# Kernel optimization log

Hardware: AMD Instinct MI355X
Metric: run time of the kernel (lower is better)

Reference implementation:

```python
import jax, jax.numpy as jnp
import numpy as np

TOP_K = 2  # num_experts_per_tok


def setup_inputs() -> dict:
    key = jax.random.key(0)
    ks = jax.random.split(key, 5)
    B, S, D, M, E = 4, 2048, 2048, 2048, 8
    x = jax.random.normal(ks[0], (B, S, D), dtype=jnp.float32)
    gate_kernel = jax.random.normal(ks[1], (D, E), dtype=jnp.float32) / np.sqrt(D)
    wi_0 = jax.random.normal(ks[2], (E, D, M), dtype=jnp.float32) / np.sqrt(D)
    wi_1 = jax.random.normal(ks[3], (E, D, M), dtype=jnp.float32) / np.sqrt(D)
    wo = jax.random.normal(ks[4], (E, M, D), dtype=jnp.float32) / np.sqrt(M)
    return {"x": x, "gate_kernel": gate_kernel, "wi_0": wi_0, "wi_1": wi_1, "wo": wo}


def reference(x, gate_kernel, wi_0, wi_1, wo):
    E = gate_kernel.shape[-1]
    # Gate logits: (B, S, E)
    gate_logits = jnp.einsum("bsd,de->bse", x, gate_kernel)
    # Top-k routing, then softmax over the selected experts' logits
    top_k_weights, top_k_indices = jax.lax.top_k(gate_logits, TOP_K)
    top_k_weights = jax.nn.softmax(top_k_weights.astype(jnp.float32), axis=-1).astype(x.dtype)
    # Dense combine weights per expert: (B, S, E)
    combine_w = jnp.sum(
        jax.nn.one_hot(top_k_indices, E, dtype=x.dtype) * top_k_weights[..., None], axis=-2
    )
    # Grouped GEMM (dense-masked form, as in MaxText dense_matmul path)
    h0 = jnp.einsum("bsd,edm->bsem", x, wi_0)  # (B, S, E, M)
    h1 = jnp.einsum("bsd,edm->bsem", x, wi_1)
    h = jax.nn.silu(h0) * h1 * combine_w[..., None]
    out = jnp.einsum("bsem,emd->bsd", h, wo)  # (B, S, D)
    return out
```

## Files before the change

kernel.cpp:

```cpp
#include <hip/hip_runtime.h>
#include <hip/hip_bf16.h>
#include <stdint.h>

#define TT   8192
#define DD   2048
#define MM   2048
#define NE   8

typedef float f32x4 __attribute__((ext_vector_type(4)));
typedef short s16x8 __attribute__((ext_vector_type(8)));
typedef unsigned int u32;
typedef unsigned long long u64;

static __device__ __forceinline__ short f2bf(float f) {
  __hip_bfloat16 h = __float2bfloat16(f);
  short s;
  __builtin_memcpy(&s, &h, 2);
  return s;
}
static __device__ __forceinline__ float bf2f(short s) {
  u32 u = ((u32)(unsigned short)s) << 16;
  float f;
  __builtin_memcpy(&f, &u, 4);
  return f;
}

static __device__ __forceinline__ void gload_lds16(const short* g, short* lds) {
  __builtin_amdgcn_global_load_lds(
      (const __attribute__((address_space(1))) u32*)g,
      (__attribute__((address_space(3))) u32*)lds, 16, 0, 0);
}

#define VM2()  asm volatile("s_waitcnt vmcnt(2)" ::: "memory")
#define VM0()  asm volatile("s_waitcnt vmcnt(0)" ::: "memory")
#define LG0()  asm volatile("s_waitcnt lgkmcnt(0)" ::: "memory")
#define BAR()  __builtin_amdgcn_s_barrier()

__global__ __launch_bounds__(256) void tcvt_kernel(
    const float* __restrict__ w0, const float* __restrict__ w1, const float* __restrict__ w2,
    short* __restrict__ o0, short* __restrict__ o1, short* __restrict__ o2) {
  __shared__ short tile[64][65];
  const int bz = blockIdx.z;
  const float* in; short* out;
  if (bz < 8)       { in = w0; out = o0; }
  else if (bz < 16) { in = w1; out = o1; }
  else              { in = w2; out = o2; }
  const int ex = bz & 7;
  const float* src = in + (size_t)ex * DD * MM;
  short* dst = out + (size_t)ex * DD * MM;
  const int r0 = blockIdx.y * 64;
  const int c0 = blockIdx.x * 64;
  const int t = threadIdx.x;
  const int rr = t >> 4, cc = (t & 15) * 4;
  #pragma unroll
  for (int i = 0; i < 4; i++) {
    int row = rr + i * 16;
    f32x4 v = *(const f32x4*)(src + (size_t)(r0 + row) * MM + c0 + cc);
    tile[cc + 0][row] = f2bf(v[0]);
    tile[cc + 1][row] = f2bf(v[1]);
    tile[cc + 2][row] = f2bf(v[2]);
    tile[cc + 3][row] = f2bf(v[3]);
  }
  __syncthreads();
  const int orow = t >> 2, c8 = (t & 3) * 16;
  s16x8 v0, v1;
  #pragma unroll
  for (int i = 0; i < 8; i++) { v0[i] = tile[orow][c8 + i]; v1[i] = tile[orow][c8 + 8 + i]; }
  short* dp = dst + (size_t)(c0 + orow) * DD + r0 + c8;
  *(s16x8*)(dp) = v0;
  *(s16x8*)(dp + 8) = v1;
}

__global__ __launch_bounds__(256) void gate_kernel(const float* __restrict__ x,
    const float* __restrict__ gk, int* __restrict__ counts,
    int* __restrict__ tkidx, float* __restrict__ tkw, short* __restrict__ xbf) {
  int t = blockIdx.x;
  const float* xr = x + (size_t)t * DD;
  const int d0 = threadIdx.x * 8;
  f32x4 a = *(const f32x4*)(xr + d0);
  f32x4 b = *(const f32x4*)(xr + d0 + 4);
  s16x8 v;
  v[0]=f2bf(a[0]); v[1]=f2bf(a[1]); v[2]=f2bf(a[2]); v[3]=f2bf(a[3]);
  v[4]=f2bf(b[0]); v[5]=f2bf(b[1]); v[6]=f2bf(b[2]); v[7]=f2bf(b[3]);
  *(s16x8*)(xbf + (size_t)t * DD + d0) = v;

  float acc[NE];
  #pragma unroll
  for (int e = 0; e < NE; e++) acc[e] = 0.f;
  #pragma unroll
  for (int j = 0; j < 8; j++) {
    float xv = (j < 4) ? a[j] : b[j - 4];
    const float* g = gk + (size_t)(d0 + j) * NE;
    #pragma unroll
    for (int e = 0; e < NE; e++) acc[e] += xv * g[e];
  }
  #pragma unroll
  for (int e = 0; e < NE; e++) {
    #pragma unroll
    for (int off = 32; off >= 1; off >>= 1)
      acc[e] += __shfl_xor(acc[e], off, 64);
  }
  __shared__ float red[4][NE];
  int wid = threadIdx.x >> 6;
  int lane = threadIdx.x & 63;
  if (lane == 0) {
    #pragma unroll
    for (int e = 0; e < NE; e++) red[wid][e] = acc[e];
  }
  __syncthreads();
  if (threadIdx.x == 0) {
    float l[NE];
    #pragma unroll
    for (int e = 0; e < NE; e++) l[e] = red[0][e] + red[1][e] + red[2][e] + red[3][e];
    int i1 = 0; float v1 = l[0];
    #pragma unroll
    for (int e = 1; e < NE; e++) if (l[e] > v1) { v1 = l[e]; i1 = e; }
    int i2 = -1; float v2 = -1e30f;
    #pragma unroll
    for (int e = 0; e < NE; e++) if (e != i1 && l[e] > v2) { v2 = l[e]; i2 = e; }
    float p = __expf(v2 - v1);
    float inv = 1.f / (1.f + p);
    tkidx[t*2]   = i1; tkidx[t*2+1] = i2;
    tkw[t*2]     = inv; tkw[t*2+1]  = p * inv;
    atomicAdd(&counts[i1], 1);
    atomicAdd(&counts[i2], 1);
  }
}

__global__ __launch_bounds__(256) void scatter_kernel(const int* __restrict__ counts,
    int* __restrict__ offsets, const int* __restrict__ tkidx,
    const float* __restrict__ tkw, int* __restrict__ ltok, float* __restrict__ lwt,
    int* __restrict__ slots) {
  const int e = blockIdx.x;
  const int tid = threadIdx.x;
  const int wid = tid >> 6, lane = tid & 63;
  __shared__ int base_s;
  __shared__ int wsum[4];
  if (tid == 0) {
    int s = 0;
    #pragma unroll
    for (int i = 0; i < NE; i++) {
      if (e == 0) offsets[i] = s;
      if (i < e) s += counts[i];
      else if (e == 0) s += counts[i];
    }
    if (e == 0) offsets[NE] = s;
    int bs = 0;
    for (int i = 0; i < e; i++) bs += counts[i];
    base_s = bs;
  }
  __syncthreads();
  int base = base_s;
  for (int it = 0; it < (TT * 2) / 256; it++) {
    int i = it * 256 + tid;
    bool m = (tkidx[i] == e);
    u64 b = __ballot(m);
    if (lane == 0) wsum[wid] = __popcll(b);
    __syncthreads();
    int pre = 0;
    #pragma unroll
    for (int w = 0; w < 4; w++) if (w < wid) pre += wsum[w];
    int tot = wsum[0] + wsum[1] + wsum[2] + wsum[3];
    int rank = __popcll(b & ((lane == 0) ? 0ull : ((1ull << lane) - 1ull)));
    if (m) {
      int dst = base + pre + rank;
      ltok[dst] = i >> 1;
      lwt[dst]  = tkw[i];
      slots[i]  = dst;
    }
    __syncthreads();
    base += tot;
  }
}

__global__ __launch_bounds__(256) void combine_kernel(const short* __restrict__ comb,
    const int* __restrict__ slots, float* __restrict__ out) {
  const int t = blockIdx.x;
  const int s0 = slots[2 * t], s1 = slots[2 * t + 1];
  const int idx = threadIdx.x;
  s16x8 a = *(const s16x8*)(comb + (size_t)s0 * DD + idx * 8);
  s16x8 b = *(const s16x8*)(comb + (size_t)s1 * DD + idx * 8);
  f32x4 o0, o1;
  #pragma unroll
  for (int j = 0; j < 4; j++) {
    o0[j] = bf2f(a[j]) + bf2f(b[j]);
    o1[j] = bf2f(a[4 + j]) + bf2f(b[4 + j]);
  }
  float* po = out + (size_t)t * DD + idx * 8;
  *(f32x4*)(po) = o0;
  *(f32x4*)(po + 4) = o1;
}

__device__ __forceinline__ void find_seg(const int* __restrict__ offsets, int tile, int bm,
                                         int& e, int& row0, int& rows, int& seg) {
  e = -1; row0 = 0; rows = 0; seg = 0;
  int accT = 0, prev = offsets[0];
  #pragma unroll
  for (int i = 0; i < NE; i++) {
    int nxt = offsets[i+1];
    int cnt = nxt - prev;
    int nt = (cnt + bm - 1) / bm;
    if (e < 0 && tile < accT + nt) { e = i; row0 = (tile - accT) * bm; rows = cnt; seg = prev; }
    accT += nt; prev = nxt;
  }
}

__device__ __forceinline__ void xcd_map(int ypx, int& tile, int& nyi) {
  const int bid = blockIdx.y * gridDim.x + blockIdx.x;
  const int xcd = bid & 7;
  const int i = bid >> 3;
  tile = i / ypx;
  nyi  = xcd * ypx + (i % ypx);
}

#define MAXT1 136

__global__ __launch_bounds__(256, 2) void gemm1_fast(
    const short* __restrict__ xbf,
    const short* __restrict__ w0t, const short* __restrict__ w1t,
    const int* __restrict__ offsets,
    const int* __restrict__ ltok, const float* __restrict__ lwt,
    short* __restrict__ hbuf) {
  __shared__ short As[128 * 64];
  __shared__ short B0s[128 * 64];
  __shared__ short B1s[128 * 64];
  __shared__ float w_s[128];

  int tile, nyi;
  xcd_map(2, tile, nyi);
  const int n0 = nyi * 128;
  int e, row0, rows, seg;
  find_seg(offsets, tile, 128, e, row0, rows, seg);
  if (e < 0) return;

  const int tid = threadIdx.x;
  const int lane = tid & 63, wid = tid >> 6;
  if (tid < 128) {
    int gr = row0 + tid;
    w_s[tid] = (gr < rows) ? lwt[seg + gr] : 0.f;
  }

  const int swz = ((lane & 7) ^ (lane >> 3)) * 8;
  const short* abase[4];
  const short* b0base[4];
  const short* b1base[4];
  #pragma unroll
  for (int c = 0; c < 4; c++) {
    int chunk = wid * 4 + c;
    int r = chunk * 8 + (lane >> 3);
    int gr = row0 + r; if (gr >= rows) gr = rows - 1;
    int tok = ltok[seg + gr];
    abase[c]  = xbf + (size_t)tok * DD + swz;
    int n = n0 + r;
    b0base[c] = w0t + ((size_t)e * MM + n) * DD + swz;
    b1base[c] = w1t + ((size_t)e * MM + n) * DD + swz;
  }

  const int wr = wid >> 1, wc = wid & 1;
  const int lr = lane & 15;
  const int kq = (lane >> 4) * 8;

  f32x4 acc0[4][4], acc1[4][4];
  #pragma unroll
  for (int i = 0; i < 4; i++)
    #pragma unroll
    for (int j = 0; j < 4; j++) { acc0[i][j] = 0.f; acc1[i][j] = 0.f; }

  for (int k0 = 0; k0 < DD; k0 += 64) {
    #pragma unroll
    for (int c = 0; c < 4; c++) {
      int chunk = wid * 4 + c;
      gload_lds16(abase[c]  + k0, As  + chunk * 512);
      gload_lds16(b0base[c] + k0, B0s + chunk * 512);
      gload_lds16(b1base[c] + k0, B1s + chunk * 512);
    }
    __syncthreads();

    #pragma unroll
    for (int ks = 0; ks < 2; ks++) {
      s16x8 a[4], b0[4], b1[4];
      #pragma unroll
      for (int mi = 0; mi < 4; mi++) {
        int row = wr * 64 + mi * 16 + lr;
        int koff = (ks * 32 + kq) ^ ((row & 7) * 8);
        a[mi] = *(const s16x8*)&As[row * 64 + koff];
      }
      #pragma unroll
      for (int ni = 0; ni < 4; ni++) {
        int row = wc * 64 + ni * 16 + lr;
        int koff = (ks * 32 + kq) ^ ((row & 7) * 8);
        b0[ni] = *(const s16x8*)&B0s[row * 64 + koff];
        b1[ni] = *(const s16x8*)&B1s[row * 64 + koff];
      }
      #pragma unroll
      for (int mi = 0; mi < 4; mi++)
        #pragma unroll
        for (int ni = 0; ni < 4; ni++) {
          acc0[mi][ni] = __builtin_amdgcn_mfma_f32_16x16x32_bf16(a[mi], b0[ni], acc0[mi][ni], 0, 0, 0);
          acc1[mi][ni] = __builtin_amdgcn_mfma_f32_16x16x32_bf16(a[mi], b1[ni], acc1[mi][ni], 0, 0, 0);
        }
    }
    __syncthreads();
  }

  const int lq = lane >> 4;
  #pragma unroll
  for (int mi = 0; mi < 4; mi++) {
    #pragma unroll
    for (int jj = 0; jj < 4; jj++) {
      int r = wr * 64 + mi * 16 + lq * 4 + jj;
      int gr = row0 + r;
      if (gr < rows) {
        float wgt = w_s[r];
        size_t hrow = (size_t)(seg + gr) * MM + n0;
        #pragma unroll
        for (int ni = 0; ni < 4; ni++) {
          int c = wc * 64 + ni * 16 + lr;
          float g = acc0[mi][ni][jj];
          float u = acc1[mi][ni][jj];
          float act = g / (1.f + __expf(-g));
          hbuf[hrow + c] = f2bf(act * u * wgt);
        }
      }
    }
  }
}

#define MAXT2 72

__global__ __launch_bounds__(512, 2) void gemm2_fast(
    const short* __restrict__ hbuf,
    const short* __restrict__ wot,
    const int* __restrict__ offsets,
    short* __restrict__ comb) {
  __shared__ short As[2][256 * 64];
  __shared__ short Bs[2][256 * 64];

  int tile, nyi;
  xcd_map(1, tile, nyi);
  const int n0 = nyi * 256;
  int e, row0, rows, seg;
  find_seg(offsets, tile, 256, e, row0, rows, seg);
  if (e < 0) return;

  const int tid = threadIdx.x;
  const int lane = tid & 63, wid = tid >> 6;
  const int srow = tid >> 3;
  const int swz = ((tid & 7) ^ (srow & 7)) * 8;

  const short* aP[2][2];
  const short* bP[2][2];
  #pragma unroll
  for (int h = 0; h < 2; h++)
    #pragma unroll
    for (int rd = 0; rd < 2; rd++) {
      int gr = row0 + h * 128 + rd * 64 + srow;
      if (gr >= rows) gr = rows - 1;
      aP[h][rd] = hbuf + (size_t)(seg + gr) * MM + swz;
      int n = n0 + h * 128 + rd * 64 + srow;
      bP[h][rd] = wot + ((size_t)e * DD + n) * MM + swz;
    }
  const short* aP00 = aP[0][0]; const short* aP01 = aP[0][1];
  const short* aP10 = aP[1][0]; const short* aP11 = aP[1][1];
  const short* bP00 = bP[0][0]; const short* bP01 = bP[0][1];
  const short* bP10 = bP[1][0]; const short* bP11 = bP[1][1];

  const int wr = wid >> 2, wn = wid & 3;
  const int lr = lane & 15;
  const int kq = (lane >> 4) * 8;
  const int lq = lane >> 4;

  f32x4 acc[8][4];
  #pragma unroll
  for (int i = 0; i < 8; i++)
    #pragma unroll
    for (int j = 0; j < 4; j++) acc[i][j] = 0.f;

  int brow_[4], bkey_[4];
  #pragma unroll
  for (int ni = 0; ni < 4; ni++) {
    brow_[ni] = wn * 64 + ni * 16 + lr;
    bkey_[ni] = (brow_[ni] & 7) * 8;
  }
  int arowL_[4], akeyL_[4], arowH_[4], akeyH_[4];
  #pragma unroll
  for (int mi = 0; mi < 4; mi++) {
    arowL_[mi] = wr * 128 + mi * 16 + lr;        akeyL_[mi] = (arowL_[mi] & 7) * 8;
    arowH_[mi] = wr * 128 + (mi + 4) * 16 + lr;  akeyH_[mi] = (arowH_[mi] & 7) * 8;
  }

  const int wofs = wid * 512;
  auto stA0 = [&](int buf, int kof) {
    short* d = &As[buf][0];
    gload_lds16(aP00 + kof, d + wofs);
    gload_lds16(aP01 + kof, d + 4096 + wofs);
  };
  auto stA1 = [&](int buf, int kof) {
    short* d = &As[buf][128 * 64];
    gload_lds16(aP10 + kof, d + wofs);
    gload_lds16(aP11 + kof, d + 4096 + wofs);
  };
  auto stB0 = [&](int buf, int kof) {
    short* d = &Bs[buf][0];
    gload_lds16(bP00 + kof, d + wofs);
    gload_lds16(bP01 + kof, d + 4096 + wofs);
  };
  auto stB1 = [&](int buf, int kof) {
    short* d = &Bs[buf][128 * 64];
    gload_lds16(bP10 + kof, d + wofs);
    gload_lds16(bP11 + kof, d + 4096 + wofs);
  };

  stA0(0, 0); stB0(0, 0); stB1(0, 0); stA1(0, 0);
  stA0(1, 64);
  VM2();
  BAR();

  const int NIT = (MM / 64) / 2;
  s16x8 av[4], bv[4], bw[4];

  for (int it = 0; it < NIT; ++it) {
    const bool pf = (it + 1 < NIT);
    const int kb  = (2 * it + 1) * 64;
    const int kna = (2 * it + 2) * 64;
    const int knb = (2 * it + 3) * 64;

    #pragma unroll
    for (int mi = 0; mi < 4; mi++) av[mi] = *(const s16x8*)&As[0][arowL_[mi] * 64 + (kq ^ akeyL_[mi])];
    #pragma unroll
    for (int ni = 0; ni < 4; ni++) bv[ni] = *(const s16x8*)&Bs[0][brow_[ni] * 64 + (kq ^ bkey_[ni])];
    stB0(1, kb);
    BAR(); LG0();
    __builtin_amdgcn_s_setprio(1);
    #pragma unroll
    for (int mi = 0; mi < 4; mi++)
      #pragma unroll
      for (int ni = 0; ni < 4; ni++)
        acc[mi][ni] = __builtin_amdgcn_mfma_f32_16x16x32_bf16(av[mi], bv[ni], acc[mi][ni], 0, 0, 0);
    __builtin_amdgcn_s_setprio(0);
    BAR();

    #pragma unroll
    for (int mi = 0; mi < 4; mi++) av[mi] = *(const s16x8*)&As[0][arowH_[mi] * 64 + (kq ^ akeyH_[mi])];
    stB1(1, kb);
    BAR(); LG0();
    __builtin_amdgcn_s_setprio(1);
    #pragma unroll
    for (int mi = 0; mi < 4; mi++)
      #pragma unroll
      for (int ni = 0; ni < 4; ni++)
        acc[mi + 4][ni] = __builtin_amdgcn_mfma_f32_16x16x32_bf16(av[mi], bv[ni], acc[mi + 4][ni], 0, 0, 0);
    __builtin_amdgcn_s_setprio(0);
    BAR();

    #pragma unroll
    for (int mi = 0; mi < 4; mi++) av[mi] = *(const s16x8*)&As[0][arowL_[mi] * 64 + ((32 + kq) ^ akeyL_[mi])];
    #pragma unroll
    for (int ni = 0; ni < 4; ni++) bw[ni] = *(const s16x8*)&Bs[0][brow_[ni] * 64 + ((32 + kq) ^ bkey_[ni])];
    stA1(1, kb);
    BAR(); LG0();
    __builtin_amdgcn_s_setprio(1);
    #pragma unroll
    for (int mi = 0; mi < 4; mi++)
      #pragma unroll
      for (int ni = 0; ni < 4; ni++)
        acc[mi][ni] = __builtin_amdgcn_mfma_f32_16x16x32_bf16(av[mi], bw[ni], acc[mi][ni], 0, 0, 0);
    __builtin_amdgcn_s_setprio(0);
    BAR();

    #pragma unroll
    for (int mi = 0; mi < 4; mi++) av[mi] = *(const s16x8*)&As[0][arowH_[mi] * 64 + ((32 + kq) ^ akeyH_[mi])];
    if (pf) stA0(0, kna);
    BAR(); LG0();
    __builtin_amdgcn_s_setprio(1);
    #pragma unroll
    for (int mi = 0; mi < 4; mi++)
      #pragma unroll
      for (int ni = 0; ni < 4; ni++)
        acc[mi + 4][ni] = __builtin_amdgcn_mfma_f32_16x16x32_bf16(av[mi], bw[ni], acc[mi + 4][ni], 0, 0, 0);
    __builtin_amdgcn_s_setprio(0);
    if (pf) { VM2(); } else { VM0(); }
    BAR();

    #pragma unroll
    for (int mi = 0; mi < 4; mi++) av[mi] = *(const s16x8*)&As[1][arowL_[mi] * 64 + (kq ^ akeyL_[mi])];
    #pragma unroll
    for (int ni = 0; ni < 4; ni++) bv[ni] = *(const s16x8*)&Bs[1][brow_[ni] * 64 + (kq ^ bkey_[ni])];
    if (pf) stB0(0, kna);
    BAR(); LG0();
    __builtin_amdgcn_s_setprio(1);
    #pragma unroll
    for (int mi = 0; mi < 4; mi++)
      #pragma unroll
      for (int ni = 0; ni < 4; ni++)
        acc[mi][ni] = __builtin_amdgcn_mfma_f32_16x16x32_bf16(av[mi], bv[ni], acc[mi][ni], 0, 0, 0);
    __builtin_amdgcn_s_setprio(0);
    BAR();

    #pragma unroll
    for (int mi = 0; mi < 4; mi++) av[mi] = *(const s16x8*)&As[1][arowH_[mi] * 64 + (kq ^ akeyH_[mi])];
    if (pf) stB1(0, kna);
    BAR(); LG0();
    __builtin_amdgcn_s_setprio(1);
    #pragma unroll
    for (int mi = 0; mi < 4; mi++)
      #pragma unroll
      for (int ni = 0; ni < 4; ni++)
        acc[mi + 4][ni] = __builtin_amdgcn_mfma_f32_16x16x32_bf16(av[mi], bv[ni], acc[mi + 4][ni], 0, 0, 0);
    __builtin_amdgcn_s_setprio(0);
    BAR();

    #pragma unroll
    for (int mi = 0; mi < 4; mi++) av[mi] = *(const s16x8*)&As[1][arowL_[mi] * 64 + ((32 + kq) ^ akeyL_[mi])];
    #pragma unroll
    for (int ni = 0; ni < 4; ni++) bw[ni] = *(const s16x8*)&Bs[1][brow_[ni] * 64 + ((32 + kq) ^ bkey_[ni])];
    if (pf) stA1(0, kna);
    BAR(); LG0();
    __builtin_amdgcn_s_setprio(1);
    #pragma unroll
    for (int mi = 0; mi < 4; mi++)
      #pragma unroll
      for (int ni = 0; ni < 4; ni++)
        acc[mi][ni] = __builtin_amdgcn_mfma_f32_16x16x32_bf16(av[mi], bw[ni], acc[mi][ni], 0, 0, 0);
    __builtin_amdgcn_s_setprio(0);
    BAR();

    #pragma unroll
    for (int mi = 0; mi < 4; mi++) av[mi] = *(const s16x8*)&As[1][arowH_[mi] * 64 + ((32 + kq) ^ akeyH_[mi])];
    if (pf) stA0(1, knb);
    BAR(); LG0();
    __builtin_amdgcn_s_setprio(1);
    #pragma unroll
    for (int mi = 0; mi < 4; mi++)
      #pragma unroll
      for (int ni = 0; ni < 4; ni++)
        acc[mi + 4][ni] = __builtin_amdgcn_mfma_f32_16x16x32_bf16(av[mi], bw[ni], acc[mi + 4][ni], 0, 0, 0);
    __builtin_amdgcn_s_setprio(0);
    if (pf) { VM2(); BAR(); }
  }

  #pragma unroll
  for (int mi = 0; mi < 8; mi++) {
    #pragma unroll
    for (int jj = 0; jj < 4; jj++) {
      int r = wr * 128 + mi * 16 + lq * 4 + jj;
      int gr = row0 + r;
      if (gr < rows) {
        size_t orow = (size_t)(seg + gr) * DD + n0;
        #pragma unroll
        for (int ni = 0; ni < 4; ni++) {
          int c = wn * 64 + ni * 16 + lr;
          comb[orow + c] = f2bf(acc[mi][ni][jj]);
        }
      }
    }
  }
}

extern "C" void kernel_launch(void* const* d_in, const int* in_sizes, int n_in,
                              void* d_out, int out_size, void* d_ws, size_t ws_size,
                              hipStream_t stream) {
  const float* x   = (const float*)d_in[0];
  const float* gk  = (const float*)d_in[1];
  const float* wi0 = (const float*)d_in[2];
  const float* wi1 = (const float*)d_in[3];
  const float* wo  = (const float*)d_in[4];
  float* out = (float*)d_out;

  char* w = (char*)d_ws;
  int*   counts  = (int*)(w);
  int*   offsets = (int*)(w + 256);
  int*   tkidx   = (int*)(w + 1024);
  float* tkw     = (float*)(w + 1024 + 65536);
  int*   ltok    = (int*)(w + 1024 + 2*65536);
  float* lwt     = (float*)(w + 1024 + 3*65536);
  int*   slots   = (int*)(w + 1024 + 4*65536);
  short* xbf  = (short*)(w + 524288);
  short* hbuf = xbf + (size_t)TT * DD;
  short* w0t  = hbuf + (size_t)2 * TT * MM;
  short* w1t  = w0t + (size_t)NE * DD * MM;
  short* wot  = w1t + (size_t)NE * DD * MM;
  short* comb = w0t;

  hipMemsetAsync(counts, 0, 64, stream);

  gate_kernel<<<TT, 256, 0, stream>>>(x, gk, counts, tkidx, tkw, xbf);
  scatter_kernel<<<NE, 256, 0, stream>>>(counts, offsets, tkidx, tkw, ltok, lwt, slots);
  tcvt_kernel<<<dim3(MM/64, DD/64, 24), 256, 0, stream>>>(wi0, wi1, wo, w0t, w1t, wot);

  gemm1_fast<<<dim3(MAXT1, MM/128), 256, 0, stream>>>(xbf, w0t, w1t, offsets, ltok, lwt, hbuf);
  gemm2_fast<<<dim3(MAXT2, DD/256), 512, 0, stream>>>(hbuf, wot, offsets, comb);
  combine_kernel<<<TT, 256, 0, stream>>>(comb, slots, out);
}
```

Before: 890.7 us.

## Fold wo weight conversion into gemm1 launch to overlap with GEMM

The fp32-to-bf16 transpose-convert of wo moves out of the standalone conversion kernel and into extra blocks appended to the gemm1 grid. Those blocks use the A shared-memory buffer as a transpose tile and then return. The aim is to overlap the memory-bound wo conversion with the compute-bound first grouped GEMM, which also runs partly as a tail for early-exiting gemm1 blocks. The 2D grid becomes 1D, so the XCD mapping is recomputed inline. Since conversion blocks come after the GEMM blocks in the grid, they may only get scheduled late and could still compete for bandwidth and slots.

```diff
diff --git a/kernel.cpp b/kernel.cpp
--- a/kernel.cpp
+++ b/kernel.cpp
@@ -36,15 +36,13 @@
 #define LG0()  asm volatile("s_waitcnt lgkmcnt(0)" ::: "memory")
 #define BAR()  __builtin_amdgcn_s_barrier()
 
-__global__ __launch_bounds__(256) void tcvt_kernel(
-    const float* __restrict__ w0, const float* __restrict__ w1, const float* __restrict__ w2,
-    short* __restrict__ o0, short* __restrict__ o1, short* __restrict__ o2) {
+__global__ __launch_bounds__(256) void tcvt01_kernel(
+    const float* __restrict__ w0, const float* __restrict__ w1,
+    short* __restrict__ o0, short* __restrict__ o1) {
   __shared__ short tile[64][65];
   const int bz = blockIdx.z;
-  const float* in; short* out;
-  if (bz < 8)       { in = w0; out = o0; }
-  else if (bz < 16) { in = w1; out = o1; }
-  else              { in = w2; out = o2; }
+  const float* in  = (bz < 8) ? w0 : w1;
+  short* out       = (bz < 8) ? o0 : o1;
   const int ex = bz & 7;
   const float* src = in + (size_t)ex * DD * MM;
   short* dst = out + (size_t)ex * DD * MM;
@@ -213,21 +211,58 @@
   nyi  = xcd * ypx + (i % ypx);
 }
 
-#define MAXT1 136
-
-__global__ __launch_bounds__(256, 2) void gemm1_fast(
+#define G1TILES 136
+#define G1GRID  (G1TILES * 16)
+#define GOGRID  (8 * 32 * 32)
+
+__global__ __launch_bounds__(256, 2) void gemm1_fused(
     const short* __restrict__ xbf,
     const short* __restrict__ w0t, const short* __restrict__ w1t,
     const int* __restrict__ offsets,
     const int* __restrict__ ltok, const float* __restrict__ lwt,
-    short* __restrict__ hbuf) {
+    short* __restrict__ hbuf,
+    const float* __restrict__ wo, short* __restrict__ wot) {
   __shared__ short As[128 * 64];
   __shared__ short B0s[128 * 64];
   __shared__ short B1s[128 * 64];
   __shared__ float w_s[128];
 
-  int tile, nyi;
-  xcd_map(2, tile, nyi);
+  const int bid = blockIdx.x;
+  if (bid >= G1GRID) {
+    short (*tile)[65] = (short(*)[65])As;
+    const int idx = bid - G1GRID;
+    const int ex = idx >> 10;
+    const int rem = idx & 1023;
+    const int r0 = (rem >> 5) * 64;
+    const int c0 = (rem & 31) * 64;
+    const float* src = wo + (size_t)ex * DD * MM;
+    short* dst = wot + (size_t)ex * DD * MM;
+    const int t = threadIdx.x;
+    const int rr = t >> 4, cc = (t & 15) * 4;
+    #pragma unroll
+    for (int i = 0; i < 4; i++) {
+      int row = rr + i * 16;
+      f32x4 v = *(const f32x4*)(src + (size_t)(r0 + row) * MM + c0 + cc);
+      tile[cc + 0][row] = f2bf(v[0]);
+      tile[cc + 1][row] = f2bf(v[1]);
+      tile[cc + 2][row] = f2bf(v[2]);
+      tile[cc + 3][row] = f2bf(v[3]);
+    }
+    __syncthreads();
+    const int orow = t >> 2, c8 = (t & 3) * 16;
+    s16x8 v0, v1;
+    #pragma unroll
+    for (int i = 0; i < 8; i++) { v0[i] = tile[orow][c8 + i]; v1[i] = tile[orow][c8 + 8 + i]; }
+    short* dp = dst + (size_t)(c0 + orow) * DD + r0 + c8;
+    *(s16x8*)(dp) = v0;
+    *(s16x8*)(dp + 8) = v1;
+    return;
+  }
+
+  const int xcd = bid & 7;
+  const int bi = bid >> 3;
+  const int tile = bi >> 1;
+  const int nyi = xcd * 2 + (bi & 1);
   const int n0 = nyi * 128;
   int e, row0, rows, seg;
   find_seg(offsets, tile, 128, e, row0, rows, seg);
@@ -586,9 +621,10 @@
 
   gate_kernel<<<TT, 256, 0, stream>>>(x, gk, counts, tkidx, tkw, xbf);
   scatter_kernel<<<NE, 256, 0, stream>>>(counts, offsets, tkidx, tkw, ltok, lwt, slots);
-  tcvt_kernel<<<dim3(MM/64, DD/64, 24), 256, 0, stream>>>(wi0, wi1, wo, w0t, w1t, wot);
-
-  gemm1_fast<<<dim3(MAXT1, MM/128), 256, 0, stream>>>(xbf, w0t, w1t, offsets, ltok, lwt, hbuf);
+  tcvt01_kernel<<<dim3(MM/64, DD/64, 16), 256, 0, stream>>>(wi0, wi1, w0t, w1t);
+
+  gemm1_fused<<<G1GRID + GOGRID, 256, 0, stream>>>(xbf, w0t, w1t, offsets, ltok, lwt,
+                                                   hbuf, wo, wot);
   gemm2_fast<<<dim3(MAXT2, DD/256), 512, 0, stream>>>(hbuf, wot, offsets, comb);
   combine_kernel<<<TT, 256, 0, stream>>>(comb, slots, out);
 }
```

Measured after the change: 855.0 us. 4.0% less time.
